# Optimization experiments

Measured on AMD Instinct MI355X. Metric: run time of the kernel, lower is better.

The kernel has to match this reference:

```python
import jax, jax.numpy as jnp
import numpy as np

B, N, C, K, KS, OC = 8, 4096, 64, 20, 16, 64


def setup_inputs() -> dict:
    key = jax.random.key(0)
    ks = jax.random.split(key, 6)
    return {
        'x': jax.random.normal(ks[0], (B, 3, N), jnp.float32),
        'feature': jax.random.normal(ks[1], (B, C, N), jnp.float32),
        'kernals': jax.random.normal(ks[2], (3, KS), jnp.float32),
        'mlp_w': jax.random.normal(ks[3], (C, 7), jnp.float32) * 0.1,
        'mlp_b': jnp.zeros((C,), jnp.float32),
        'conv_w': jax.random.normal(ks[4], (OC, 2 * C * KS), jnp.float32) * 0.02,
        'conv_b': jnp.zeros((OC,), jnp.float32),
        'bn_gamma': jnp.ones((OC,), jnp.float32),
        'bn_beta': jnp.zeros((OC,), jnp.float32),
    }


def reference(x, feature, kernals, mlp_w, mlp_b, conv_w, conv_b, bn_gamma, bn_beta):
    b, _, n = x.shape
    c = feature.shape[1]
    ksz = kernals.shape[1]
    k = K
    # ---- knn on coords ----
    xt = jnp.swapaxes(x, 1, 2)                      # [B,N,3]
    inner = -2.0 * jnp.einsum('bnc,bmc->bnm', xt, xt)
    xx = jnp.sum(xt * xt, axis=-1)                  # [B,N]
    pd = -xx[:, :, None] - inner - xx[:, None, :]   # negative squared dist
    idx = jax.lax.top_k(pd, k)[1]                   # [B,N,K] nearest (incl. self)
    gather = jax.vmap(lambda pts, i: pts[i])        # per-batch gather
    # ---- geometric features ----
    x_sp = gather(xt, idx)                          # [B,N,K,3]
    x_rel = x_sp - x_sp[:, :, 0:1, :]               # [B,N,K,3]
    x_dis = jnp.linalg.norm(x_rel, axis=-1, keepdims=True)
    center = jnp.broadcast_to(x_sp[:, :, 0:1, :], x_sp.shape)
    x_feats7 = jnp.concatenate([center, x_rel, x_dis], axis=-1)  # [B,N,K,7]
    # Conv1d(7,C,1) == pointwise linear over the 7 channels
    x_feats = jnp.einsum('bnkc,oc->bnok', x_feats7, mlp_w) + mlp_b[None, None, :, None]  # [B,N,C,K]
    # ---- neighbor feature gather ----
    ft = jnp.swapaxes(feature, 1, 2)                # [B,N,C]
    sp_f = gather(ft, idx)                          # [B,N,K,C]
    spirals = jnp.concatenate([jnp.swapaxes(sp_f, 2, 3), x_feats], axis=2)  # [B,N,2C,K]
    # ---- adjacency weights ----
    one_pad = jnp.zeros((k, ksz), jnp.float32).at[0, 0].set(1.0)
    aw = jnp.einsum('bnkc,cs->bnks', x_rel, kernals) + one_pad   # [B,N,K,KS]
    aw = jnp.where(aw > 0, aw, 0.0)
    aw = aw / (jnp.sum(aw, axis=2, keepdims=True) + 1e-6)
    aw = aw * aw
    aw = aw / (jnp.sum(aw, axis=2, keepdims=True) + 1e-6)
    aw = jnp.where(aw > 0.1, aw, 0.0)
    # ---- weighted aggregation + linear ----
    agg = jnp.einsum('bnck,bnks->bncs', spirals, aw)             # [B,N,2C,KS]
    agg = agg.reshape(b, n, 2 * c * ksz)
    out = agg @ conv_w.T + conv_b                                # [B,N,OC]
    out = jnp.swapaxes(out, 1, 2)                                # [B,OC,N]
    # ---- BatchNorm1d (training-mode batch statistics, eps=1e-5) ----
    mean = jnp.mean(out, axis=(0, 2), keepdims=True)
    var = jnp.var(out, axis=(0, 2), keepdims=True)
    out = (out - mean) / jnp.sqrt(var + 1e-5)
    out = out * bn_gamma[None, :, None] + bn_beta[None, :, None]
    return out
```

## Files before the change

kernel.cpp:

```cpp
#include <hip/hip_runtime.h>
#include <cfloat>
#include <math.h>

#define NB 8
#define NPT 4096
#define NC 64
#define KNN 20
#define KSZ 16
#define BPTS 8

typedef __attribute__((ext_vector_type(8))) short short8;
typedef __attribute__((ext_vector_type(4))) float f32x4;
typedef __attribute__((ext_vector_type(2))) float f32x2;

__device__ __forceinline__ unsigned short f2bf(float f) {
  unsigned u = __float_as_uint(f);
  unsigned r = (u + 0x7fffu + ((u >> 16) & 1u)) >> 16;
  return (unsigned short)r;
}
__device__ __forceinline__ float bf2f(unsigned short h) {
  return __uint_as_float(((unsigned)h) << 16);
}

__device__ __forceinline__ f32x2 pk_fma_zw(f32x2 a, f32x2 zw) {
  f32x2 d;
  asm("v_pk_fma_f32 %0, %1, %2, %2 op_sel:[0,0,1] op_sel_hi:[1,0,1]"
      : "=v"(d) : "v"(a), "v"(zw));
  return d;
}
__device__ __forceinline__ f32x2 pk_fma_s1hi(f32x2 a, f32x2 b, f32x2 c) {
  f32x2 d;
  asm("v_pk_fma_f32 %0, %1, %2, %3 op_sel:[0,1,0] op_sel_hi:[1,1,1]"
      : "=v"(d) : "v"(a), "v"(b), "v"(c));
  return d;
}
__device__ __forceinline__ f32x2 pk_fma_s1lo(f32x2 a, f32x2 b, f32x2 c) {
  f32x2 d;
  asm("v_pk_fma_f32 %0, %1, %2, %3 op_sel:[0,0,0] op_sel_hi:[1,0,1]"
      : "=v"(d) : "v"(a), "v"(b), "v"(c));
  return d;
}


__device__ __noinline__ void knn_full(const float4* __restrict__ pts, int n, int lane,
                                      int g, int* __restrict__ idxOut) {
  const int M = 24;
  float4 qp = pts[n];
  float qx = qp.x, qy = qp.y, qz = qp.z;
  float v[M];
  int id[M];
#pragma unroll
  for (int r = 0; r < M; ++r) { v[r] = FLT_MAX; id[r] = 0x7fffffff; }
  for (int i = 0; i < 64; ++i) {
    int j = (i << 6) | lane;
    float4 p = pts[j];
    float dx = p.x - qx, dy = p.y - qy, dz = p.z - qz;
    float d2 = fmaf(dx, dx, fmaf(dy, dy, dz * dz));
    bool c[M];
#pragma unroll
    for (int r = 0; r < M; ++r) c[r] = d2 < v[r];
#pragma unroll
    for (int r = M - 1; r >= 1; --r) {
      v[r] = c[r - 1] ? v[r - 1] : (c[r] ? d2 : v[r]);
      id[r] = c[r - 1] ? id[r - 1] : (c[r] ? j : id[r]);
    }
    v[0] = c[0] ? d2 : v[0];
    id[0] = c[0] ? j : id[0];
  }
  unsigned long long key = ((unsigned long long)__float_as_uint(v[0]) << 32) | (unsigned)id[0];
  unsigned long long ext = ~0ull;
  for (int r = 0; r < 24; ++r) {
    unsigned long long k = key;
#pragma unroll
    for (int s = 1; s < 64; s <<= 1) {
      unsigned long long o = __shfl_xor(k, s, 64);
      k = (o < k) ? o : k;
    }
    if (lane == r) ext = k;
    if (key == k) {
#pragma unroll
      for (int q = 0; q < M - 1; ++q) { v[q] = v[q + 1]; id[q] = id[q + 1]; }
      v[M - 1] = FLT_MAX;
      id[M - 1] = 0x7fffffff;
      key = ((unsigned long long)__float_as_uint(v[0]) << 32) | (unsigned)id[0];
    }
  }
  int ei = (int)(unsigned)(ext & 0xffffffffu);
  bool al = lane < 24;
  double dv = -1.0;
  if (al) {
    float4 p = pts[ei];
    double dx = (double)p.x - (double)qx;
    double dy = (double)p.y - (double)qy;
    double dz = (double)p.z - (double)qz;
    dv = dx * dx + dy * dy + dz * dz;
  }
#pragma unroll
  for (int r = 0; r < 4; ++r) {
    double bd = al ? dv : -1.0;
    int bi = al ? ei : -1;
#pragma unroll
    for (int s = 1; s < 64; s <<= 1) {
      double od = __shfl_xor(bd, s, 64);
      int oi = __shfl_xor(bi, s, 64);
      if (od > bd || (od == bd && oi > bi)) { bd = od; bi = oi; }
    }
    if (al && ei == bi) al = false;
  }
  unsigned long long msk = __ballot(al && ei != n);
  if (al) {
    if (ei == n) {
      idxOut[g * 20] = n;
    } else {
      int pos = 1 + __popcll(msk & ((1ull << lane) - 1ull));
      idxOut[g * 20 + pos] = ei;
    }
  }
}

__launch_bounds__(1024, 2)
__global__ void k_knn_prep(const float* __restrict__ x, int* __restrict__ idxOut,
                           const float* __restrict__ cw, const float* __restrict__ mlp_w,
                           const float* __restrict__ mlp_b, const float* __restrict__ f,
                           unsigned short* __restrict__ bp, unsigned short* __restrict__ bp2,
                           unsigned short* __restrict__ ft) {
  __shared__ __align__(16) unsigned char sm[66560];
  int K = blockIdx.x;

  if (K >= 512) {
    int vb = (K - 512) * 4 + (threadIdx.x >> 8);
    int vt = threadIdx.x & 255;
    if (vb < 256) {
      int t = vb * 256 + vt;
      int j = t & 7, lane = (t >> 3) & 63, nt = (t >> 9) & 3, ks = t >> 11;
      int k = ks * 32 + ((lane >> 4) << 3) + j;
      int o = nt * 16 + (lane & 15);
      bp[t] = f2bf(cw[o * 2048 + k]);
    } else if (vb < 288) {
      int t = (vb - 256) * 256 + vt;
      int jj = t & 7, lane = (t >> 3) & 63, nt = (t >> 9) & 3, ks2 = t >> 11;
      int k = ks2 * 32 + ((lane >> 4) << 3) + jj;
      int s = k >> 3, j = k & 7;
      int o = nt * 16 + (lane & 15);
      float acc = 0.0f;
      for (int c = 0; c < 64; ++c) {
        float coef = (j < 7) ? mlp_w[c * 7 + j] : mlp_b[c];
        acc = fmaf(cw[o * 2048 + 1024 + c * 16 + s], coef, acc);
      }
      bp2[t] = f2bf(acc);
    } else {
      float(*tile)[65] = (float(*)[65])(sm + (threadIdx.x >> 8) * 16640);
      int blk3 = vb - 288;
      int b = blk3 >> 6;
      int n0 = (blk3 & 63) * 64;
      int lane = vt & 63;
      int rr = vt >> 6;
#pragma unroll
      for (int c0 = 0; c0 < 64; c0 += 4) {
        int c = c0 + rr;
        tile[c][lane] = f[(b * 64 + c) * 4096 + n0 + lane];
      }
      __syncthreads();
#pragma unroll
      for (int m0 = 0; m0 < 64; m0 += 4) {
        int nn = m0 + rr;
        ft[(b * 4096 + n0 + nn) * 64 + lane] = f2bf(tile[lane][nn]);
      }
    }
    return;
  }

  float4* pts = (float4*)sm;
  int b = K >> 6;
  const float* xb = x + b * 3 * 4096;
  for (int i = threadIdx.x; i < 4096; i += 1024) {
    float px = xb[i], py = xb[4096 + i], pz = xb[8192 + i];
    pts[i] = make_float4(px, py, pz, fmaf(px, px, fmaf(py, py, pz * pz)));
  }
  __syncthreads();

  int lane = threadIdx.x & 63;
  int w = threadIdx.x >> 6;
  int nb = ((K & 63) << 6) + (w << 2);
  int gb = b * 4096 + nb;

  float4 q0 = pts[nb], q1 = pts[nb + 1], q2 = pts[nb + 2], q3 = pts[nb + 3];
  f32x2 m2x01 = {-2.0f * q0.x, -2.0f * q1.x};
  f32x2 m2y01 = {-2.0f * q0.y, -2.0f * q1.y};
  f32x2 m2z01 = {-2.0f * q0.z, -2.0f * q1.z};
  f32x2 m2x23 = {-2.0f * q2.x, -2.0f * q3.x};
  f32x2 m2y23 = {-2.0f * q2.y, -2.0f * q3.y};
  f32x2 m2z23 = {-2.0f * q2.z, -2.0f * q3.z};

  float v0 = FLT_MAX, v1 = FLT_MAX, v2 = FLT_MAX, v3 = FLT_MAX;
#pragma unroll 4
  for (int i = 0; i < 64; ++i) {
    float4 p = pts[(i << 6) | lane];
    f32x2 pxy = {p.x, p.y}, pzw = {p.z, p.w};
    f32x2 t0 = pk_fma_zw(m2z01, pzw);
    f32x2 t1 = pk_fma_zw(m2z23, pzw);
    t0 = pk_fma_s1hi(m2y01, pxy, t0);
    t1 = pk_fma_s1hi(m2y23, pxy, t1);
    t0 = pk_fma_s1lo(m2x01, pxy, t0);
    t1 = pk_fma_s1lo(m2x23, pxy, t1);
    v0 = fminf(v0, t0[0]);
    v1 = fminf(v1, t0[1]);
    v2 = fminf(v2, t1[0]);
    v3 = fminf(v3, t1[1]);
  }

#pragma unroll
  for (int k = 2; k <= 64; k <<= 1) {
#pragma unroll
    for (int j = k >> 1; j > 0; j >>= 1) {
      bool sel = ((lane & k) == 0) == ((lane & j) == 0);
      {
        float o = __shfl_xor(v0, j, 64);
        v0 = sel ? fminf(v0, o) : fmaxf(v0, o);
      }
      {
        float o = __shfl_xor(v1, j, 64);
        v1 = sel ? fminf(v1, o) : fmaxf(v1, o);
      }
      {
        float o = __shfl_xor(v2, j, 64);
        v2 = sel ? fminf(v2, o) : fmaxf(v2, o);
      }
      {
        float o = __shfl_xor(v3, j, 64);
        v3 = sel ? fminf(v3, o) : fmaxf(v3, o);
      }
    }
  }
  float T0 = __shfl(v0, 23, 64);
  float T1 = __shfl(v1, 23, 64);
  float T2 = __shfl(v2, 23, 64);
  float T3 = __shfl(v3, 23, 64);

  int ei0 = -1, ei1 = -1, ei2 = -1, ei3 = -1;
  int base0 = 0, base1 = 0, base2 = 0, base3 = 0;
  bool ovf0 = false, ovf1 = false, ovf2 = false, ovf3 = false;
#pragma unroll 2
  for (int i = 0; i < 64; ++i) {
    int j = (i << 6) | lane;
    float4 p = pts[j];
    f32x2 pxy = {p.x, p.y}, pzw = {p.z, p.w};
    f32x2 t0 = pk_fma_zw(m2z01, pzw);
    f32x2 t1 = pk_fma_zw(m2z23, pzw);
    t0 = pk_fma_s1hi(m2y01, pxy, t0);
    t1 = pk_fma_s1hi(m2y23, pxy, t1);
    t0 = pk_fma_s1lo(m2x01, pxy, t0);
    t1 = pk_fma_s1lo(m2x23, pxy, t1);
    {
      bool pred = (t0[0] <= T0);
      unsigned long long mask = __ballot(pred);
      if (mask) {
        int cnt = __popcll(mask);
        if (base0 + cnt > 63) {
          ovf0 = true;
        } else {
          int dst = pred ? (base0 + __popcll(mask & ((1ull << lane) - 1ull))) : 63;
          int got = __builtin_amdgcn_ds_permute(dst << 2, j);
          bool recv = (lane >= base0) && (lane < base0 + cnt);
          ei0 = recv ? got : ei0;
        }
        base0 += cnt;
      }
    }
    {
      bool pred = (t0[1] <= T1);
      unsigned long long mask = __ballot(pred);
      if (mask) {
        int cnt = __popcll(mask);
        if (base1 + cnt > 63) {
          ovf1 = true;
        } else {
          int dst = pred ? (base1 + __popcll(mask & ((1ull << lane) - 1ull))) : 63;
          int got = __builtin_amdgcn_ds_permute(dst << 2, j);
          bool recv = (lane >= base1) && (lane < base1 + cnt);
          ei1 = recv ? got : ei1;
        }
        base1 += cnt;
      }
    }
    {
      bool pred = (t1[0] <= T2);
      unsigned long long mask = __ballot(pred);
      if (mask) {
        int cnt = __popcll(mask);
        if (base2 + cnt > 63) {
          ovf2 = true;
        } else {
          int dst = pred ? (base2 + __popcll(mask & ((1ull << lane) - 1ull))) : 63;
          int got = __builtin_amdgcn_ds_permute(dst << 2, j);
          bool recv = (lane >= base2) && (lane < base2 + cnt);
          ei2 = recv ? got : ei2;
        }
        base2 += cnt;
      }
    }
    {
      bool pred = (t1[1] <= T3);
      unsigned long long mask = __ballot(pred);
      if (mask) {
        int cnt = __popcll(mask);
        if (base3 + cnt > 63) {
          ovf3 = true;
        } else {
          int dst = pred ? (base3 + __popcll(mask & ((1ull << lane) - 1ull))) : 63;
          int got = __builtin_amdgcn_ds_permute(dst << 2, j);
          bool recv = (lane >= base3) && (lane < base3 + cnt);
          ei3 = recv ? got : ei3;
        }
        base3 += cnt;
      }
    }
  }

  int c[4], e[4];
  c[0] = ovf0 ? 0 : base0;
  c[1] = ovf1 ? 0 : base1;
  c[2] = ovf2 ? 0 : base2;
  c[3] = ovf3 ? 0 : base3;
  e[0] = ei0;
  e[1] = ei1;
  e[2] = ei2;
  e[3] = ei3;
  int rank0 = 0, rank1 = 0, rank2 = 0, rank3 = 0;
  double dm[4];
#pragma unroll
  for (int r = 0; r < 4; ++r) {
    int e_ = (lane < c[r]) ? e[r] : 0;
    e[r] = e_;
    float4 pp = pts[e_];
    float4 qq = pts[nb + r];
    double dx = (double)pp.x - (double)qq.x;
    double dy = (double)pp.y - (double)qq.y;
    double dz = (double)pp.z - (double)qq.z;
    dm[r] = dx * dx + dy * dy + dz * dz;
  }
  int cmax = max(max(c[0], c[1]), max(c[2], c[3]));
  for (int it = 0; it < cmax; ++it) {
#pragma unroll
    for (int r = 0; r < 4; ++r) {
      int lo = __builtin_amdgcn_readlane(__double2loint(dm[r]), it);
      int hi = __builtin_amdgcn_readlane(__double2hiint(dm[r]), it);
      int ir = __builtin_amdgcn_readlane(e[r], it);
      double dr = __hiloint2double(hi, lo);
      bool less = (it < c[r]) && ((dr < dm[r]) || (dr == dm[r] && ir < e[r]));
      int inc = (lane < c[r] && less) ? 1 : 0;
      if (r == 0) rank0 += inc;
      else if (r == 1) rank1 += inc;
      else if (r == 2) rank2 += inc;
      else rank3 += inc;
    }
  }
#pragma unroll
  for (int r = 0; r < 4; ++r) {
    int rk = (r == 0) ? rank0 : (r == 1) ? rank1 : (r == 2) ? rank2 : rank3;
    bool kept = (lane < c[r]) && (rk < 20);
    bool selfk = kept && (e[r] == nb + r);
    if (__ballot(selfk) != 0ull) {
      if (kept) idxOut[(gb + r) * 20 + rk] = e[r];
    } else {
      knn_full(pts, nb + r, lane, gb + r, idxOut);
    }
  }
}

#define AGG_OFF 0
#define AWB_OFF 16384
#define FPA_OFF 24576
#define F7S_OFF 28672
#define QL_OFF  31232
#define IDX_OFF 31360
#define SMEM_SZ 33792

__launch_bounds__(256, 4)
__global__ void k_main(const float* __restrict__ x, const float* __restrict__ feat,
                       const unsigned short* __restrict__ ftT, int useFtT,
                       const float* __restrict__ kern,
                       const unsigned short* __restrict__ bpk,
                       const unsigned short* __restrict__ bpk2,
                       const float* __restrict__ conv_b, const int* __restrict__ idxIn,
                       float* __restrict__ out) {
  __shared__ __align__(16) unsigned char smem[SMEM_SZ];
  unsigned short* agg = (unsigned short*)(smem + AGG_OFF);
  unsigned short* awB = (unsigned short*)(smem + AWB_OFF);
  float4* f7s = (float4*)(smem + F7S_OFF);
  float4* qL = (float4*)(smem + QL_OFF);
  int* idxL = (int*)(smem + IDX_OFF);

  int t = threadIdx.x;
  int lane = t & 63;
  int w = t >> 6;
  int b = blockIdx.x & 7;
  int n0 = (blockIdx.x >> 3) * BPTS;
  int g0 = b * 4096 + n0;
  const float* xb = x + b * 3 * 4096;

  {
    int pt = t >> 5, slot = t & 31;
    int n = n0 + pt;
    float qx = xb[n], qy = xb[4096 + n], qz = xb[8192 + n];
    if (slot < 20) {
      int kk = idxIn[(g0 + pt) * 20 + slot];
      idxL[pt * 20 + slot] = kk;
      float rx = xb[kk] - qx, ry = xb[4096 + kk] - qy, rz = xb[8192 + kk] - qz;
      float ds = sqrtf(rx * rx + ry * ry + rz * rz);
      f7s[pt * 20 + slot] = make_float4(rx, ry, rz, ds);
    } else if (slot == 20) {
      qL[pt] = make_float4(qx, qy, qz, 0.0f);
    }
  }
  __syncthreads();

  if (t < 128) {
    int pt = t >> 4, s = t & 15;
    float kx = kern[s], ky = kern[16 + s], kz = kern[32 + s];
    float wv[20];
#pragma unroll
    for (int k = 0; k < 20; ++k) {
      float4 f = f7s[pt * 20 + k];
      float dot = f.x * kx + f.y * ky + f.z * kz;
      if (s == 0 && k == 0) dot += 1.0f;
      wv[k] = dot > 0.0f ? dot : 0.0f;
    }
    float sum = 0.0f;
#pragma unroll
    for (int k = 0; k < 20; ++k) sum += wv[k];
    float inv1 = 1.0f / (sum + 1e-6f);
    float sum2 = 0.0f;
#pragma unroll
    for (int k = 0; k < 20; ++k) {
      float u = wv[k] * inv1;
      sum2 += u * u;
    }
    float inv2 = 1.0f / (sum2 + 1e-6f);
    float colsum = 0.0f;
    float F0 = 0.0f, F1 = 0.0f, F2 = 0.0f, F3 = 0.0f;
    unsigned short* awp = awB + pt * 512;
#pragma unroll
    for (int k = 0; k < 20; ++k) {
      float u = wv[k] * inv1;
      u = u * u * inv2;
      u = (u > 0.1f) ? u : 0.0f;
      awp[(((k >> 3) * 16 + s) << 3) + (k & 7)] = f2bf(u);
      colsum += u;
      float4 f = f7s[pt * 20 + k];
      F0 = fmaf(f.x, u, F0);
      F1 = fmaf(f.y, u, F1);
      F2 = fmaf(f.z, u, F2);
      F3 = fmaf(f.w, u, F3);
    }
#pragma unroll
    for (int k = 20; k < 32; ++k)
      awp[(((k >> 3) * 16 + s) << 3) + (k & 7)] = 0;
    float4 q = qL[pt];
    __align__(16) unsigned short tmp[8];
    tmp[0] = f2bf(q.x * colsum);
    tmp[1] = f2bf(q.y * colsum);
    tmp[2] = f2bf(q.z * colsum);
    tmp[3] = f2bf(F0);
    tmp[4] = f2bf(F1);
    tmp[5] = f2bf(F2);
    tmp[6] = f2bf(F3);
    tmp[7] = f2bf(colsum);
    *(uint4*)(smem + FPA_OFF + pt * 256 + ((s ^ (pt & 7)) << 4)) = *(uint4*)tmp;
  }
  __syncthreads();

  {
    int r15 = lane & 15, chunk = lane >> 4;
#pragma unroll
    for (int half = 0; half < 2; ++half) {
      int pt = (w << 1) + half;
      int nofs[8];
#pragma unroll
      for (int j = 0; j < 8; ++j) {
        int k = (chunk << 3) + j;
        nofs[j] = (k < 20) ? ((b * 4096 + idxL[pt * 20 + k]) << 6) : -1;
      }
      short8 bfrag = *(const short8*)(awB + pt * 512 + (lane << 3));
      f32x4 accA[4];
#pragma unroll
      for (int ct = 0; ct < 4; ++ct) accA[ct] = (f32x4){0.f, 0.f, 0.f, 0.f};
#pragma unroll
      for (int ct = 0; ct < 4; ++ct) {
        int c = (ct << 4) + r15;
        union { short8 v; unsigned short u[8]; } af;
#pragma unroll
        for (int j = 0; j < 8; ++j) {
          unsigned short val = 0;
          if (nofs[j] >= 0) {
            if (useFtT) val = ftT[nofs[j] + c];
            else val = f2bf(feat[(b * 64 + c) * 4096 + (nofs[j] >> 6) - b * 4096]);
          }
          af.u[j] = val;
        }
        accA[ct] = __builtin_amdgcn_mfma_f32_16x16x32_bf16(af.v, bfrag, accA[ct], 0, 0, 0);
      }
      char* rb = (char*)(smem + AGG_OFF) + pt * 2048;
      int sw = (pt & 7) << 4;
#pragma unroll
      for (int ct = 0; ct < 4; ++ct)
#pragma unroll
        for (int q = 0; q < 4; ++q) {
          int kidx = (((ct << 4) + (chunk << 2) + q) << 4) + r15;
          *(unsigned short*)(rb + ((kidx << 1) ^ sw)) = f2bf(accA[ct][q]);
        }
    }
  }
  __syncthreads();

  f32x4 acc[4];
#pragma unroll
  for (int nt = 0; nt < 4; ++nt) acc[nt] = (f32x4){0.f, 0.f, 0.f, 0.f};
  {
    int r = lane & 15;
    const char* rowbase = (const char*)(smem + AGG_OFF) + r * 2048;
#pragma unroll
    for (int ks = 0; ks < 8; ++ks) {
      int ksl = w * 8 + ks;
      int off = (ksl * 64 + ((lane >> 4) << 4)) ^ ((r & 7) << 4);
      short8 af = *(const short8*)(rowbase + off);
#pragma unroll
      for (int nt = 0; nt < 4; ++nt) {
        short8 bf = *(const short8*)(bpk + (((ksl * 4 + nt) * 64 + lane) << 3));
        acc[nt] = __builtin_amdgcn_mfma_f32_16x16x32_bf16(af, bf, acc[nt], 0, 0, 0);
      }
    }
    {
      int chunk = (w << 2) + (lane >> 4);
      short8 af = *(const short8*)(smem + FPA_OFF + r * 256 + ((chunk ^ (r & 7)) << 4));
#pragma unroll
      for (int nt = 0; nt < 4; ++nt) {
        short8 bf = *(const short8*)(bpk2 + ((((w << 2) + nt) * 64 + lane) << 3));
        acc[nt] = __builtin_amdgcn_mfma_f32_16x16x32_bf16(af, bf, acc[nt], 0, 0, 0);
      }
    }
  }
  __syncthreads();

  float* red = (float*)(smem + AGG_OFF);
  {
#pragma unroll
    for (int nt = 0; nt < 4; ++nt)
#pragma unroll
      for (int r = 0; r < 4; ++r) {
        int row = ((lane >> 4) << 2) + r;
        if (row < 8) {
          int o = nt * 16 + (lane & 15);
          red[(w * 8 + row) * 64 + (o ^ ((row & 7) << 2))] = acc[nt][r];
        }
      }
  }
  __syncthreads();
#pragma unroll
  for (int rep = 0; rep < 2; ++rep) {
    int u = rep * 256 + t;
    int pt = u & 7, o = u >> 3;
    float s = conv_b[o];
#pragma unroll
    for (int w2 = 0; w2 < 4; ++w2) s += red[(w2 * 8 + pt) * 64 + (o ^ ((pt & 7) << 2))];
    out[(b * 64 + o) * 4096 + n0 + pt] = s;
  }
}

__global__ void k_bnstats1(const float* __restrict__ out, double* __restrict__ partial) {
  __shared__ double rs[256], rq[256];
  int o = blockIdx.x & 63, b = blockIdx.x >> 6;
  const float* p = out + (b * 64 + o) * 4096;
  double s = 0.0, q = 0.0;
  for (int i = threadIdx.x; i < 4096; i += 256) {
    double v = (double)p[i];
    s += v;
    q += v * v;
  }
  rs[threadIdx.x] = s;
  rq[threadIdx.x] = q;
  __syncthreads();
  for (int st = 128; st > 0; st >>= 1) {
    if ((int)threadIdx.x < st) {
      rs[threadIdx.x] += rs[threadIdx.x + st];
      rq[threadIdx.x] += rq[threadIdx.x + st];
    }
    __syncthreads();
  }
  if (threadIdx.x == 0) {
    partial[(o * 8 + b) * 2] = rs[0];
    partial[(o * 8 + b) * 2 + 1] = rq[0];
  }
}

__global__ void k_bnapply(float* __restrict__ out, const double* __restrict__ partial,
                          const float* __restrict__ gamma, const float* __restrict__ beta) {
  __shared__ float sc_sh[2];
  int o = (blockIdx.x >> 2) & 63;
  if (threadIdx.x == 0) {
    double s = 0.0, q = 0.0;
#pragma unroll
    for (int b = 0; b < 8; ++b) {
      s += partial[(o * 8 + b) * 2];
      q += partial[(o * 8 + b) * 2 + 1];
    }
    double mean = s / 32768.0;
    double var = q / 32768.0 - mean * mean;
    double inv = 1.0 / sqrt(var + 1e-5);
    double sc = (double)gamma[o] * inv;
    sc_sh[0] = (float)sc;
    sc_sh[1] = (float)((double)beta[o] - mean * sc);
  }
  __syncthreads();
  int i4 = blockIdx.x * 256 + threadIdx.x;
  float sc = sc_sh[0], sh = sc_sh[1];
  float4 v = ((const float4*)out)[i4];
  v.x = fmaf(v.x, sc, sh);
  v.y = fmaf(v.y, sc, sh);
  v.z = fmaf(v.z, sc, sh);
  v.w = fmaf(v.w, sc, sh);
  ((float4*)out)[i4] = v;
}

extern "C" void kernel_launch(void* const* d_in, const int* in_sizes, int n_in,
                              void* d_out, int out_size, void* d_ws, size_t ws_size,
                              hipStream_t stream) {
  const float* x = (const float*)d_in[0];
  const float* feat = (const float*)d_in[1];
  const float* kern = (const float*)d_in[2];
  const float* mlp_w = (const float*)d_in[3];
  const float* mlp_b = (const float*)d_in[4];
  const float* conv_w = (const float*)d_in[5];
  const float* conv_b = (const float*)d_in[6];
  const float* gamma = (const float*)d_in[7];
  const float* beta = (const float*)d_in[8];
  float* out = (float*)d_out;
  char* ws = (char*)d_ws;

  int* idx = (int*)ws;
  double* partial = (double*)(ws + 2621440);
  unsigned short* bpk = (unsigned short*)(ws + 2633728);
  unsigned short* bpk2 = (unsigned short*)(ws + 2764800);
  unsigned short* ftT = (unsigned short*)(ws + 2781184);
  int useFtT = (ws_size >= (size_t)(2781184 + 4194304)) ? 1 : 0;

  k_knn_prep<<<712, 1024, 0, stream>>>(x, idx, conv_w, mlp_w, mlp_b, feat,
                                       bpk, bpk2, ftT);
  k_main<<<4096, 256, 0, stream>>>(x, feat, ftT, useFtT, kern, bpk, bpk2,
                                   conv_b, idx, out);
  k_bnstats1<<<512, 256, 0, stream>>>(out, partial);
  k_bnapply<<<2048, 256, 0, stream>>>(out, partial, gamma, beta);
}
```

Baseline: 172.0 us.

## Buffer KNN candidates per lane in packed registers, compact once after scan

Inside the candidate scan loop, each lane no longer does a per-iteration ballot, popcount and ds_permute compaction for each of the four query points. It now pushes passing point indices as 16-bit fields into a 64-bit register history (up to four per lane) and counts them. A single compaction pass runs after the loop, and the code falls back to the overflow path when any lane collects more than four candidates. The launch bound occupancy hint is also raised from 2 to 8, which pressures register allocation and may cause spills.

Result: slower. 213.7 us (+24.2%).

```diff
diff --git a/kernel.cpp b/kernel.cpp
--- a/kernel.cpp
+++ b/kernel.cpp
@@ -118,7 +118,7 @@
   }
 }
 
-__launch_bounds__(1024, 2)
+__launch_bounds__(1024, 8)
 __global__ void k_knn_prep(const float* __restrict__ x, int* __restrict__ idxOut,
                            const float* __restrict__ cw, const float* __restrict__ mlp_w,
                            const float* __restrict__ mlp_b, const float* __restrict__ f,
@@ -237,9 +237,8 @@
   float T2 = __shfl(v2, 23, 64);
   float T3 = __shfl(v3, 23, 64);
 
-  int ei0 = -1, ei1 = -1, ei2 = -1, ei3 = -1;
-  int base0 = 0, base1 = 0, base2 = 0, base3 = 0;
-  bool ovf0 = false, ovf1 = false, ovf2 = false, ovf3 = false;
+  unsigned long long h0 = 0ull, h1 = 0ull, h2 = 0ull, h3 = 0ull;
+  int c0 = 0, c1 = 0, c2 = 0, c3 = 0;
 #pragma unroll 2
   for (int i = 0; i < 64; ++i) {
     int j = (i << 6) | lane;
@@ -252,80 +251,55 @@
     t0 = pk_fma_s1lo(m2x01, pxy, t0);
     t1 = pk_fma_s1lo(m2x23, pxy, t1);
     {
-      bool pred = (t0[0] <= T0);
-      unsigned long long mask = __ballot(pred);
-      if (mask) {
-        int cnt = __popcll(mask);
-        if (base0 + cnt > 63) {
-          ovf0 = true;
-        } else {
-          int dst = pred ? (base0 + __popcll(mask & ((1ull << lane) - 1ull))) : 63;
-          int got = __builtin_amdgcn_ds_permute(dst << 2, j);
-          bool recv = (lane >= base0) && (lane < base0 + cnt);
-          ei0 = recv ? got : ei0;
-        }
-        base0 += cnt;
-      }
+      bool pr = (t0[0] <= T0);
+      h0 = pr ? ((h0 << 16) | (unsigned long long)(unsigned)j) : h0;
+      c0 += pr;
     }
     {
-      bool pred = (t0[1] <= T1);
-      unsigned long long mask = __ballot(pred);
-      if (mask) {
-        int cnt = __popcll(mask);
-        if (base1 + cnt > 63) {
-          ovf1 = true;
-        } else {
-          int dst = pred ? (base1 + __popcll(mask & ((1ull << lane) - 1ull))) : 63;
-          int got = __builtin_amdgcn_ds_permute(dst << 2, j);
-          bool recv = (lane >= base1) && (lane < base1 + cnt);
-          ei1 = recv ? got : ei1;
-        }
-        base1 += cnt;
-      }
+      bool pr = (t0[1] <= T1);
+      h1 = pr ? ((h1 << 16) | (unsigned long long)(unsigned)j) : h1;
+      c1 += pr;
     }
     {
-      bool pred = (t1[0] <= T2);
-      unsigned long long mask = __ballot(pred);
-      if (mask) {
-        int cnt = __popcll(mask);
-        if (base2 + cnt > 63) {
-          ovf2 = true;
-        } else {
-          int dst = pred ? (base2 + __popcll(mask & ((1ull << lane) - 1ull))) : 63;
-          int got = __builtin_amdgcn_ds_permute(dst << 2, j);
-          bool recv = (lane >= base2) && (lane < base2 + cnt);
-          ei2 = recv ? got : ei2;
-        }
-        base2 += cnt;
-      }
+      bool pr = (t1[0] <= T2);
+      h2 = pr ? ((h2 << 16) | (unsigned long long)(unsigned)j) : h2;
+      c2 += pr;
     }
     {
-      bool pred = (t1[1] <= T3);
-      unsigned long long mask = __ballot(pred);
-      if (mask) {
-        int cnt = __popcll(mask);
-        if (base3 + cnt > 63) {
-          ovf3 = true;
-        } else {
-          int dst = pred ? (base3 + __popcll(mask & ((1ull << lane) - 1ull))) : 63;
-          int got = __builtin_amdgcn_ds_permute(dst << 2, j);
-          bool recv = (lane >= base3) && (lane < base3 + cnt);
-          ei3 = recv ? got : ei3;
-        }
-        base3 += cnt;
-      }
+      bool pr = (t1[1] <= T3);
+      h3 = pr ? ((h3 << 16) | (unsigned long long)(unsigned)j) : h3;
+      c3 += pr;
     }
   }
 
   int c[4], e[4];
-  c[0] = ovf0 ? 0 : base0;
-  c[1] = ovf1 ? 0 : base1;
-  c[2] = ovf2 ? 0 : base2;
-  c[3] = ovf3 ? 0 : base3;
-  e[0] = ei0;
-  e[1] = ei1;
-  e[2] = ei2;
-  e[3] = ei3;
+  {
+    unsigned long long hs[4] = {h0, h1, h2, h3};
+    int cn[4] = {c0, c1, c2, c3};
+#pragma unroll
+    for (int r = 0; r < 4; ++r) {
+      bool bad = (__ballot(cn[r] > 4) != 0ull);
+      int base = 0, ev = 0;
+#pragma unroll
+      for (int s = 1; s <= 4; ++s) {
+        unsigned long long ms = __ballot(cn[r] >= s);
+        int pc = __popcll(ms);
+        bool part = cn[r] >= s;
+        int sh = ((cn[r] - s) << 4) & 63;
+        int val = (int)((hs[r] >> sh) & 0xffffull);
+        int dst = part ? (base + __popcll(ms & ((1ull << lane) - 1ull))) : 63;
+        dst = dst > 63 ? 63 : dst;
+        int got = __builtin_amdgcn_ds_permute(dst << 2, val);
+        bool recv = (lane >= base) && (lane < base + pc);
+        ev = recv ? got : ev;
+        base += pc;
+      }
+      bad = bad || (base > 63);
+      c[r] = bad ? 0 : base;
+      e[r] = ev;
+    }
+  }
+
   int rank0 = 0, rank1 = 0, rank2 = 0, rank3 = 0;
   double dm[4];
 #pragma unroll
```
